# Performance work log

Measured on AMD Instinct MI355X. Metric: run time of the kernel, lower is better.

Reference implementation:

```python
import jax, jax.numpy as jnp
import numpy as np
import math

E = 1024
H = 16
D = E // H  # head_dim = 64


def setup_inputs() -> dict:
    key = jax.random.key(0)
    ks = jax.random.split(key, 12)
    B, N = 2, 2048
    x = jax.random.normal(ks[0], (B, N, E), dtype=jnp.float32)
    region_mask = jax.random.randint(ks[1], (B, N), 0, 2).astype(jnp.float32)
    attn_mask = jax.random.randint(ks[2], (B, N, N), 0, 2).astype(bool)
    std = 0.02
    Wq = jax.random.normal(ks[3], (E, E), dtype=jnp.float32) * std
    Wk = jax.random.normal(ks[4], (E, E), dtype=jnp.float32) * std
    Wv = jax.random.normal(ks[5], (E, E), dtype=jnp.float32) * std
    Wo = jax.random.normal(ks[6], (E, E), dtype=jnp.float32) * std
    bq = jnp.zeros((E,), jnp.float32)
    bk = jnp.zeros((E,), jnp.float32)
    bv = jnp.zeros((E,), jnp.float32)
    bo = jnp.zeros((E,), jnp.float32)
    region_bias = jax.random.normal(ks[7], (1, H, 1, 1), dtype=jnp.float32) * std
    return {"x": x, "region_mask": region_mask, "attn_mask": attn_mask,
            "Wq": Wq, "bq": bq, "Wk": Wk, "bk": bk, "Wv": Wv, "bv": bv,
            "Wo": Wo, "bo": bo, "region_bias": region_bias}


def reference(x, region_mask, attn_mask, Wq, bq, Wk, bk, Wv, bv, Wo, bo, region_bias):
    B, N, _ = x.shape
    # projections (torch Linear: y = x @ W.T + b), split heads -> (B, H, N, D)
    def split_heads(y):
        return y.reshape(B, N, H, D).transpose(0, 2, 1, 3)
    q = split_heads(x @ Wq.T + bq)
    k = split_heads(x @ Wk.T + bk)
    v = split_heads(x @ Wv.T + bv)
    # eager scores (B, H, N, N)
    scores = jnp.einsum('bhqd,bhkd->bhqk', q, k) / math.sqrt(D)
    # additive regional bias: (1,H,1,1) * (B,1,N,1) broadcasts over keys
    scores = scores + region_bias * region_mask[:, None, :, None]
    # masked_fill(attn_mask, -inf); mask is (B,N,N) -> (B,1,N,N)
    scores = jnp.where(attn_mask[:, None, :, :], -jnp.inf, scores)
    w = jax.nn.softmax(scores, axis=-1)  # dropout is identity in eval
    out = jnp.einsum('bhqk,bhkd->bhqd', w, v)
    out = out.transpose(0, 2, 1, 3).reshape(B, N, E)
    return out @ Wo.T + bo
```

## Files before the change

### kernel.cpp

```cpp
#include <hip/hip_runtime.h>
#include <hip/hip_bf16.h>
#include <stdint.h>

typedef __hip_bfloat16 bf16;
typedef unsigned long long u64;
typedef __attribute__((ext_vector_type(4))) float f32x4;
typedef __attribute__((ext_vector_type(8))) short short8;

#define MFMA16 __builtin_amdgcn_mfma_f32_16x16x32_bf16

constexpr int Bc = 2, Nc = 2048, Ec = 1024, Hc = 16, Dc = 64;
constexpr int Mc = Bc * Nc;
constexpr int Kc = Ec;

constexpr size_t OFF_XB   = 256;
constexpr size_t SZ_XE    = (size_t)Mc * Ec * 2;
constexpr size_t SZ_W     = (size_t)Ec * Ec * 2;
constexpr size_t OFF_WQB  = OFF_XB  + SZ_XE;
constexpr size_t OFF_WKB  = OFF_WQB + SZ_W;
constexpr size_t OFF_WVB  = OFF_WKB + SZ_W;
constexpr size_t OFF_WOB  = OFF_WVB + SZ_W;
constexpr size_t OFF_QB   = OFF_WOB + SZ_W;
constexpr size_t OFF_KB   = OFF_QB  + SZ_XE;
constexpr size_t OFF_VTB  = OFF_KB  + SZ_XE;
constexpr size_t OFF_OB   = OFF_VTB + SZ_XE;
constexpr size_t OFF_MP   = OFF_OB  + SZ_XE;

#define QSCALE 0.18033688f

__device__ __forceinline__ void gld16(const void* g, void* l) {
  __builtin_amdgcn_global_load_lds((const __attribute__((address_space(1))) void*)g,
                                   (__attribute__((address_space(3))) void*)l,
                                   16, 0, 0);
}

__device__ __forceinline__ float fexp2(float x) {
#if __has_builtin(__builtin_amdgcn_exp2f)
  return __builtin_amdgcn_exp2f(x);
#else
  float r; asm("v_exp_f32 %0, %1" : "=v"(r) : "v"(x)); return r;
#endif
}

__device__ __forceinline__ unsigned cvt2(float a, float b) {
  __hip_bfloat162 h = __float22bfloat162_rn(float2{a, b});
  return *reinterpret_cast<unsigned*>(&h);
}

__device__ __forceinline__ unsigned nib4(unsigned x) {
  const unsigned b = ((x & 0x7F7F7F7Fu) + 0x7F7F7F7Fu) | x;
  return ((b >> 7) & 1u) | ((b >> 14) & 2u) | ((b >> 21) & 4u) | ((b >> 28) & 8u);
}

__global__ __launch_bounds__(256)
void prep(const unsigned char* __restrict__ mbytes,
          const float* __restrict__ x,  const float* __restrict__ wq,
          const float* __restrict__ wk, const float* __restrict__ wv,
          const float* __restrict__ wo,
          u64* __restrict__ packed,
          uint2* __restrict__ xb,  uint2* __restrict__ wqb,
          uint2* __restrict__ wkb, uint2* __restrict__ wvb,
          uint2* __restrict__ wob)
{
  if (blockIdx.x < 512) {
    __shared__ int found;
    if (threadIdx.x == 0) found = 0;
    __syncthreads();
    int loc = 0;
    for (int i = threadIdx.x; i < 4096; i += 256)
      if ((i & 3) && mbytes[i] == 1) loc = 1;
    if (loc) atomicOr(&found, 1);
    __syncthreads();
    const bool bytem = (found != 0);

    const int widx = blockIdx.x * 256 + threadIdx.x;
    u64 bits = 0;
    if (bytem) {
      const uint4* src = (const uint4*)(mbytes + (size_t)widx * 64);
#pragma unroll
      for (int i = 0; i < 4; ++i) {
        const uint4 v = src[i];
        bits |= (u64)nib4(v.x) << (16 * i + 0);
        bits |= (u64)nib4(v.y) << (16 * i + 4);
        bits |= (u64)nib4(v.z) << (16 * i + 8);
        bits |= (u64)nib4(v.w) << (16 * i + 12);
      }
    } else {
      const uint4* src = (const uint4*)mbytes + (size_t)widx * 16;
#pragma unroll
      for (int i = 0; i < 16; ++i) {
        const uint4 v = src[i];
        const unsigned n = (v.x != 0 ? 1u : 0u) | (v.y != 0 ? 2u : 0u) |
                           (v.z != 0 ? 4u : 0u) | (v.w != 0 ? 8u : 0u);
        bits |= (u64)n << (4 * i);
      }
    }
    packed[widx] = bits;
    return;
  }
  const long XG = (long)Mc * Ec / 4;
  const long WG = (long)Ec * Ec / 4;
  const long total = XG + 4 * WG;
  const long nthr = (long)(gridDim.x - 512) * 256;
  for (long g = (long)(blockIdx.x - 512) * 256 + threadIdx.x; g < total; g += nthr) {
    const float* src; uint2* dst; long r;
    if (g < XG)              { src = x;  dst = xb;  r = g; }
    else if (g < XG + WG)    { src = wq; dst = wqb; r = g - XG; }
    else if (g < XG + 2*WG)  { src = wk; dst = wkb; r = g - XG - WG; }
    else if (g < XG + 3*WG)  { src = wv; dst = wvb; r = g - XG - 2*WG; }
    else                     { src = wo; dst = wob; r = g - XG - 3*WG; }
    float4 v = reinterpret_cast<const float4*>(src)[r];
    uint2 o;
    o.x = cvt2(v.x, v.y);
    o.y = cvt2(v.z, v.w);
    dst[r] = o;
  }
}

__global__ __launch_bounds__(256)
void gemm_qkv(const bf16* __restrict__ xb,
              const bf16* __restrict__ wq, const bf16* __restrict__ wk,
              const bf16* __restrict__ wv,
              const float* __restrict__ bq, const float* __restrict__ bk,
              const float* __restrict__ bv,
              bf16* __restrict__ Q, bf16* __restrict__ Ko, bf16* __restrict__ VT)
{
  __shared__ bf16 As[2][128 * 64];
  __shared__ bf16 Bs[2][3][64 * 64];
  const int bm = blockIdx.x >> 4, bn = blockIdx.x & 15;
  const int t = threadIdx.x, lane = t & 63, w = t >> 6;
  const int wr = w >> 1, wc = w & 1;
  const int llo = lane & 15, lhi = lane >> 4;
  const int srow = t >> 3, schunk = t & 7;
  const int sswz = schunk ^ (srow & 7);
  const bf16* aSrc  = xb + (size_t)(bm * 128 + srow) * Kc + sswz * 8;
  const bf16* bSrc0 = wq + (size_t)(bn * 64 + srow) * Kc + sswz * 8;
  const bf16* bSrc1 = wk + (size_t)(bn * 64 + srow) * Kc + sswz * 8;
  const bf16* bSrc2 = wv + (size_t)(bn * 64 + srow) * Kc + sswz * 8;

  f32x4 acc[3][4][2] = {};

  auto stage = [&](int buf, int kt) {
    char* ldsA = (char*)As[buf] + w * 1024;
#pragma unroll
    for (int i = 0; i < 4; ++i)
      gld16(aSrc + (size_t)i * 32 * Kc + kt, ldsA + i * 4096);
#pragma unroll
    for (int s = 0; s < 3; ++s) {
      const bf16* bs = s == 0 ? bSrc0 : (s == 1 ? bSrc1 : bSrc2);
      char* ldsB = (char*)Bs[buf][s] + w * 1024;
      gld16(bs + kt, ldsB);
      gld16(bs + (size_t)32 * Kc + kt, ldsB + 4096);
    }
  };

  stage(0, 0);
  __syncthreads();

  for (int kti = 0; kti < Kc / 64; ++kti) {
    const int cur = kti & 1;
    if (kti + 1 < Kc / 64) stage(cur ^ 1, (kti + 1) * 64);
    const char* Asc = (const char*)As[cur];
#pragma unroll
    for (int kk = 0; kk < 2; ++kk) {
      const int chunk = (kk * 4 + lhi) ^ (lane & 7);
      short8 af[4];
#pragma unroll
      for (int i = 0; i < 4; ++i) {
        const int rowa = wr * 64 + i * 16 + llo;
        af[i] = *(const short8*)(Asc + rowa * 128 + chunk * 16);
      }
#pragma unroll
      for (int s = 0; s < 3; ++s) {
        const char* Bsc = (const char*)Bs[cur][s];
        const int rowb0 = wc * 32 + llo;
        short8 bg0 = *(const short8*)(Bsc + rowb0 * 128 + chunk * 16);
        short8 bg1 = *(const short8*)(Bsc + (rowb0 + 16) * 128 + chunk * 16);
#pragma unroll
        for (int i = 0; i < 4; ++i) {
          acc[s][i][0] = MFMA16(af[i], bg0, acc[s][i][0], 0, 0, 0);
          acc[s][i][1] = MFMA16(af[i], bg1, acc[s][i][1], 0, 0, 0);
        }
      }
    }
    __syncthreads();
  }

#pragma unroll
  for (int s = 0; s < 3; ++s) {
    const float* bias = s == 0 ? bq : (s == 1 ? bk : bv);
#pragma unroll
    for (int i = 0; i < 4; ++i)
#pragma unroll
      for (int j = 0; j < 2; ++j)
#pragma unroll
        for (int r = 0; r < 4; ++r) {
          const int m = bm * 128 + wr * 64 + i * 16 + lhi * 4 + r;
          const int e = bn * 64 + wc * 32 + j * 16 + llo;
          float v = acc[s][i][j][r] + bias[e];
          if (s == 0) {
            Q[(size_t)m * Ec + e] = __float2bfloat16(v * QSCALE);
          } else if (s == 1) {
            Ko[(size_t)m * Ec + e] = __float2bfloat16(v);
          } else {
            const int b = m >> 11, n = m & 2047, h = e >> 6, d = e & 63;
            VT[(((size_t)(b * Hc + h)) * Dc + d) * Nc + n] = __float2bfloat16(v);
          }
        }
  }
}

__global__ __launch_bounds__(256)
void gemm_out(const bf16* __restrict__ ob, const bf16* __restrict__ wo,
              const float* __restrict__ bo, float* __restrict__ out)
{
  __shared__ bf16 As[2][64 * 64], Bs[2][64 * 64];
  const int bm = blockIdx.x >> 4, bn = blockIdx.x & 15;
  const int t = threadIdx.x, lane = t & 63, w = t >> 6;
  const int wr = w >> 1, wc = w & 1;
  const int llo = lane & 15, lhi = lane >> 4;
  const int srow = t >> 3, schunk = t & 7;
  const int sswz = schunk ^ (srow & 7);
  const bf16* aSrc = ob + (size_t)(bm * 64 + srow) * Kc + sswz * 8;
  const bf16* bSrc = wo + (size_t)(bn * 64 + srow) * Kc + sswz * 8;

  f32x4 acc[2][2] = {};

  auto stage = [&](int buf, int kt) {
    gld16(aSrc + kt,                     (char*)As[buf] + w * 1024);
    gld16(aSrc + (size_t)32 * Kc + kt,   (char*)As[buf] + 4096 + w * 1024);
    gld16(bSrc + kt,                     (char*)Bs[buf] + w * 1024);
    gld16(bSrc + (size_t)32 * Kc + kt,   (char*)Bs[buf] + 4096 + w * 1024);
  };

  stage(0, 0);
  __syncthreads();

  for (int kti = 0; kti < Kc / 64; ++kti) {
    const int cur = kti & 1;
    if (kti + 1 < Kc / 64) stage(cur ^ 1, (kti + 1) * 64);
    const char* Asc = (const char*)As[cur];
    const char* Bsc = (const char*)Bs[cur];
#pragma unroll
    for (int kk = 0; kk < 2; ++kk) {
      const int chunk = (kk * 4 + lhi) ^ (lane & 7);
      short8 af[2], bg[2];
#pragma unroll
      for (int i = 0; i < 2; ++i) {
        const int rowa = wr * 32 + i * 16 + llo;
        af[i] = *(const short8*)(Asc + rowa * 128 + chunk * 16);
      }
#pragma unroll
      for (int j = 0; j < 2; ++j) {
        const int rowb = wc * 32 + j * 16 + llo;
        bg[j] = *(const short8*)(Bsc + rowb * 128 + chunk * 16);
      }
#pragma unroll
      for (int i = 0; i < 2; ++i)
#pragma unroll
        for (int j = 0; j < 2; ++j)
          acc[i][j] = MFMA16(af[i], bg[j], acc[i][j], 0, 0, 0);
    }
    __syncthreads();
  }

#pragma unroll
  for (int i = 0; i < 2; ++i)
#pragma unroll
    for (int j = 0; j < 2; ++j)
#pragma unroll
      for (int r = 0; r < 4; ++r) {
        const int m = bm * 64 + wr * 32 + i * 16 + lhi * 4 + r;
        const int e = bn * 64 + wc * 32 + j * 16 + llo;
        out[(size_t)m * Ec + e] = acc[i][j][r] + bo[e];
      }
}

__global__ __launch_bounds__(512, 4)
void flash_attn(const bf16* __restrict__ Q, const bf16* __restrict__ Kb,
                const bf16* __restrict__ VT, const u64* __restrict__ mpack,
                bf16* __restrict__ O)
{
  __shared__ bf16 Ks[2][64 * 64];
  __shared__ bf16 Vs[2][64 * 64];
  __shared__ bf16 Ps[8][2][16 * 64];
  constexpr int NT = Nc / 64;
  const int t = threadIdx.x, lane = t & 63, w = t >> 6;
  const int bh = blockIdx.x & 31, qt = blockIdx.x >> 5;
  const int b = bh >> 4, h = bh & 15;
  const int q0 = qt * 128 + w * 16;
  const int llo = lane & 15, lhi = lane >> 4;
  const int swz = (lane & 7) << 4;

  short8 aq0, aq1;
  {
    const bf16* qb = Q + ((size_t)(b * Nc + q0 + llo)) * Ec + h * Dc + lhi * 8;
    aq0 = *(const short8*)qb;
    aq1 = *(const short8*)(qb + 32);
  }

  const short8 kOnes = {16256,16256,16256,16256,16256,16256,16256,16256};
  const f32x4 fz = {};
  f32x4 oacc[4] = {};
  f32x4 lacc = {};

  const int srow = t >> 3, schunk = t & 7;
  const int sswz = schunk ^ (srow & 7);
  const bf16* kSrc = Kb + ((size_t)(b * Nc + srow)) * Ec + h * Dc + sswz * 8;
  const bf16* vSrc = VT + ((size_t)(bh * Dc + srow)) * Nc + sswz * 8;

  const u64* mrow = mpack + ((size_t)(b * Nc) + q0 + llo) * (Nc / 64);

  auto stageK = [&](int buf, int kt) {
    gld16(kSrc + (size_t)kt * Ec, (char*)Ks[buf] + w * 1024);
  };
  auto stageV = [&](int buf, int kt) {
    gld16(vSrc + kt, (char*)Vs[buf] + w * 1024);
  };

  char* pw0 = (char*)Ps[w][0] + llo * 128;
  char* pw1 = (char*)Ps[w][1] + llo * 128;

  auto qk_part = [&](const char* KsC, char* pwW, u64 mw) {
    f32x4 s[4];
    __builtin_amdgcn_s_setprio(1);
#pragma unroll
    for (int f = 0; f < 4; ++f) {
      const int row = f * 16 + llo;
      short8 kb0 = *(const short8*)(KsC + row * 128 + (((0 + lhi) * 16) ^ swz));
      short8 kb1 = *(const short8*)(KsC + row * 128 + (((4 + lhi) * 16) ^ swz));
      s[f] = MFMA16(kb0, aq0, fz, 0, 0, 0);
      s[f] = MFMA16(kb1, aq1, s[f], 0, 0, 0);
    }
    __builtin_amdgcn_s_setprio(0);

    const unsigned mlo = (unsigned)(mw >> (lhi * 4));
    const unsigned mhi = (unsigned)(mw >> (lhi * 4 + 32));
#pragma unroll
    for (int f = 0; f < 4; ++f) {
      const unsigned mf = (f < 2 ? (mlo >> (f * 16)) : (mhi >> ((f - 2) * 16)));
#pragma unroll
      for (int r = 0; r < 4; ++r) {
        const float p = fexp2(s[f][r]);
        s[f][r] = ((mf >> r) & 1u) ? 0.f : p;
      }
    }

#pragma unroll
    for (int f = 0; f < 4; ++f) {
      uint2 pk;
      pk.x = cvt2(s[f][0], s[f][1]);
      pk.y = cvt2(s[f][2], s[f][3]);
      *(uint2*)(pwW + ((f * 32 + lhi * 8) ^ swz)) = pk;
    }
  };

  auto pv_part = [&](const char* pwR, const char* VsC) {
    short8 pa0 = *(const short8*)(pwR + ((0 * 64 + lhi * 16) ^ swz));
    short8 pa1 = *(const short8*)(pwR + ((1 * 64 + lhi * 16) ^ swz));
    __builtin_amdgcn_s_setprio(1);
#pragma unroll
    for (int df = 0; df < 4; ++df) {
      const int row = df * 16 + llo;
      short8 vb0 = *(const short8*)(VsC + row * 128 + (((0 + lhi) * 16) ^ swz));
      short8 vb1 = *(const short8*)(VsC + row * 128 + (((4 + lhi) * 16) ^ swz));
      oacc[df] = MFMA16(pa0, vb0, oacc[df], 0, 0, 0);
      oacc[df] = MFMA16(pa1, vb1, oacc[df], 0, 0, 0);
    }
    lacc = MFMA16(pa0, kOnes, lacc, 0, 0, 0);
    lacc = MFMA16(pa1, kOnes, lacc, 0, 0, 0);
    __builtin_amdgcn_s_setprio(0);
  };

  stageK(0, 0);
  __syncthreads();

  stageK(1, 64);
  stageV(0, 0);
  qk_part((const char*)Ks[0], pw0, mrow[0]);
  __syncthreads();

  for (int ti = 1; ti + 1 < NT; ti += 2) {
    stageK(0, (ti + 1) * 64);
    stageV(1, ti * 64);
    pv_part(pw0, (const char*)Vs[0]);
    qk_part((const char*)Ks[1], pw1, mrow[ti]);
    __syncthreads();
    if (ti + 2 < NT) stageK(1, (ti + 2) * 64);
    stageV(0, (ti + 1) * 64);
    pv_part(pw1, (const char*)Vs[1]);
    qk_part((const char*)Ks[0], pw0, mrow[ti + 1]);
    __syncthreads();
  }

  stageV(1, (NT - 1) * 64);
  pv_part(pw0, (const char*)Vs[0]);
  qk_part((const char*)Ks[1], pw1, mrow[NT - 1]);
  __syncthreads();

  pv_part(pw1, (const char*)Vs[1]);

  float inv[4];
#pragma unroll
  for (int r = 0; r < 4; ++r) inv[r] = 1.0f / lacc[r];
#pragma unroll
  for (int df = 0; df < 4; ++df)
#pragma unroll
    for (int r = 0; r < 4; ++r) {
      const int q = q0 + lhi * 4 + r;
      const int e = h * Dc + df * 16 + llo;
      O[((size_t)(b * Nc + q)) * Ec + e] = __float2bfloat16(oacc[df][r] * inv[r]);
    }
}

extern "C" void kernel_launch(void* const* d_in, const int* in_sizes, int n_in,
                              void* d_out, int out_size, void* d_ws, size_t ws_size,
                              hipStream_t stream)
{
  (void)in_sizes; (void)n_in; (void)out_size; (void)ws_size;
  const float* x  = (const float*)d_in[0];
  const void* mask = d_in[2];
  const float* Wq = (const float*)d_in[3];
  const float* bq = (const float*)d_in[4];
  const float* Wk = (const float*)d_in[5];
  const float* bk = (const float*)d_in[6];
  const float* Wv = (const float*)d_in[7];
  const float* bv = (const float*)d_in[8];
  const float* Wo = (const float*)d_in[9];
  const float* bo = (const float*)d_in[10];
  float* out = (float*)d_out;
  char* ws = (char*)d_ws;

  bf16* XB  = (bf16*)(ws + OFF_XB);
  bf16* WQB = (bf16*)(ws + OFF_WQB);
  bf16* WKB = (bf16*)(ws + OFF_WKB);
  bf16* WVB = (bf16*)(ws + OFF_WVB);
  bf16* WOB = (bf16*)(ws + OFF_WOB);
  bf16* QB  = (bf16*)(ws + OFF_QB);
  bf16* KB  = (bf16*)(ws + OFF_KB);
  bf16* VTB = (bf16*)(ws + OFF_VTB);
  bf16* OB  = (bf16*)(ws + OFF_OB);
  u64*  MP  = (u64*)(ws + OFF_MP);

  prep<<<512 + 1280, 256, 0, stream>>>((const unsigned char*)mask,
                                       x, Wq, Wk, Wv, Wo, MP,
                                       (uint2*)XB, (uint2*)WQB, (uint2*)WKB,
                                       (uint2*)WVB, (uint2*)WOB);
  gemm_qkv<<<512, 256, 0, stream>>>(XB, WQB, WKB, WVB, bq, bk, bv, QB, KB, VTB);
  flash_attn<<<512, 512, 0, stream>>>(QB, KB, VTB, MP, OB);
  gemm_out<<<1024, 256, 0, stream>>>(OB, WOB, bo, out);
}
```

Baseline: 129.0 us.

## Load V fragments directly from global into registers, dropping V LDS staging

Removes the shared-memory staging buffers for V. Each wave now loads its V MFMA operands straight from global memory into registers and issues that load before the QK step, so the global latency can overlap with QK compute. The PV step moves after QK. This cuts LDS traffic and footprint, but every one of the 8 waves reloads the same V tile from global/L2, which adds redundant memory traffic and register pressure.

```diff
diff --git a/kernel.cpp b/kernel.cpp
--- a/kernel.cpp
+++ b/kernel.cpp
@@ -282,7 +282,6 @@
                 bf16* __restrict__ O)
 {
   __shared__ bf16 Ks[2][64 * 64];
-  __shared__ bf16 Vs[2][64 * 64];
   __shared__ bf16 Ps[8][2][16 * 64];
   constexpr int NT = Nc / 64;
   const int t = threadIdx.x, lane = t & 63, w = t >> 6;
@@ -307,15 +306,23 @@
   const int srow = t >> 3, schunk = t & 7;
   const int sswz = schunk ^ (srow & 7);
   const bf16* kSrc = Kb + ((size_t)(b * Nc + srow)) * Ec + h * Dc + sswz * 8;
-  const bf16* vSrc = VT + ((size_t)(bh * Dc + srow)) * Nc + sswz * 8;
+
+  const bf16* vBase = VT + ((size_t)bh * Dc + llo) * Nc + lhi * 8;
 
   const u64* mrow = mpack + ((size_t)(b * Nc) + q0 + llo) * (Nc / 64);
 
   auto stageK = [&](int buf, int kt) {
     gld16(kSrc + (size_t)kt * Ec, (char*)Ks[buf] + w * 1024);
   };
-  auto stageV = [&](int buf, int kt) {
-    gld16(vSrc + kt, (char*)Vs[buf] + w * 1024);
+
+  short8 vf[8];
+  auto vload = [&](int kt) {
+#pragma unroll
+    for (int df = 0; df < 4; ++df) {
+      const bf16* vp = vBase + (size_t)(df * 16) * Nc + kt;
+      vf[df * 2 + 0] = *(const short8*)vp;
+      vf[df * 2 + 1] = *(const short8*)(vp + 32);
+    }
   };
 
   char* pw0 = (char*)Ps[w][0] + llo * 128;
@@ -355,17 +362,14 @@
     }
   };
 
-  auto pv_part = [&](const char* pwR, const char* VsC) {
+  auto pv_part = [&](const char* pwR) {
     short8 pa0 = *(const short8*)(pwR + ((0 * 64 + lhi * 16) ^ swz));
     short8 pa1 = *(const short8*)(pwR + ((1 * 64 + lhi * 16) ^ swz));
     __builtin_amdgcn_s_setprio(1);
 #pragma unroll
     for (int df = 0; df < 4; ++df) {
-      const int row = df * 16 + llo;
-      short8 vb0 = *(const short8*)(VsC + row * 128 + (((0 + lhi) * 16) ^ swz));
-      short8 vb1 = *(const short8*)(VsC + row * 128 + (((4 + lhi) * 16) ^ swz));
-      oacc[df] = MFMA16(pa0, vb0, oacc[df], 0, 0, 0);
-      oacc[df] = MFMA16(pa1, vb1, oacc[df], 0, 0, 0);
+      oacc[df] = MFMA16(pa0, vf[df * 2 + 0], oacc[df], 0, 0, 0);
+      oacc[df] = MFMA16(pa1, vf[df * 2 + 1], oacc[df], 0, 0, 0);
     }
     lacc = MFMA16(pa0, kOnes, lacc, 0, 0, 0);
     lacc = MFMA16(pa1, kOnes, lacc, 0, 0, 0);
@@ -376,29 +380,29 @@
   __syncthreads();
 
   stageK(1, 64);
-  stageV(0, 0);
   qk_part((const char*)Ks[0], pw0, mrow[0]);
   __syncthreads();
 
   for (int ti = 1; ti + 1 < NT; ti += 2) {
+    vload((ti - 1) * 64);
     stageK(0, (ti + 1) * 64);
-    stageV(1, ti * 64);
-    pv_part(pw0, (const char*)Vs[0]);
     qk_part((const char*)Ks[1], pw1, mrow[ti]);
-    __syncthreads();
+    pv_part(pw0);
+    __syncthreads();
+    vload(ti * 64);
     if (ti + 2 < NT) stageK(1, (ti + 2) * 64);
-    stageV(0, (ti + 1) * 64);
-    pv_part(pw1, (const char*)Vs[1]);
     qk_part((const char*)Ks[0], pw0, mrow[ti + 1]);
-    __syncthreads();
-  }
-
-  stageV(1, (NT - 1) * 64);
-  pv_part(pw0, (const char*)Vs[0]);
+    pv_part(pw1);
+    __syncthreads();
+  }
+
+  vload((NT - 2) * 64);
   qk_part((const char*)Ks[1], pw1, mrow[NT - 1]);
+  pv_part(pw0);
   __syncthreads();
 
-  pv_part(pw1, (const char*)Vs[1]);
+  vload((NT - 1) * 64);
+  pv_part(pw1);
 
   float inv[4];
 #pragma unroll
```

Measured after the change: 214.5 us. +66.2%, slower.
